# Optimization experiments

Measured on AMD Instinct MI355X. Metric: run time of the kernel, lower is better.

Reference implementation:

```python
import jax, jax.numpy as jnp
import numpy as np

IN_C, HID, OUT_C = 768, 568, 1024
EPS = 1e-5

def _ln(x, g, b):
    mu = jnp.mean(x, axis=-1, keepdims=True)
    var = jnp.var(x, axis=-1, keepdims=True)
    return (x - mu) / jnp.sqrt(var + EPS) * g + b

def setup_inputs() -> dict:
    key = jax.random.key(0)
    ks = jax.random.split(key, 20)
    def lin(k, fan_in, fan_out):
        bound = 1.0 / np.sqrt(fan_in)
        kw, kb = jax.random.split(k)
        w = jax.random.uniform(kw, (fan_in, fan_out), jnp.float32, -bound, bound)
        b = jax.random.uniform(kb, (fan_out,), jnp.float32, -bound, bound)
        return w, b
    x = jax.random.normal(ks[0], (4, 2048, IN_C), jnp.float32)
    w_mlp, b_mlp = lin(ks[1], IN_C, HID)
    wq, bq = lin(ks[2], HID, OUT_C)
    wk, bk = lin(ks[3], HID, OUT_C)
    wv, bv = lin(ks[4], HID, OUT_C)
    wm, bm = lin(ks[5], HID, OUT_C)
    wf1, bf1 = lin(ks[6], OUT_C, OUT_C)
    wf2, bf2 = lin(ks[7], OUT_C, OUT_C)
    g1 = jnp.ones((OUT_C,), jnp.float32); be1 = jnp.zeros((OUT_C,), jnp.float32)
    g2 = jnp.ones((OUT_C,), jnp.float32); be2 = jnp.zeros((OUT_C,), jnp.float32)
    return dict(x=x, w_mlp=w_mlp, b_mlp=b_mlp, wq=wq, bq=bq, wk=wk, bk=bk,
                wv=wv, bv=bv, wm=wm, bm=bm, g1=g1, be1=be1,
                wf1=wf1, bf1=bf1, wf2=wf2, bf2=bf2, g2=g2, be2=be2)

def reference(x, w_mlp, b_mlp, wq, bq, wk, bk, wv, bv, wm, bm,
              g1, be1, wf1, bf1, wf2, bf2, g2, be2):
    # Joint.mlp: Linear + ReLU  -> h: [B, S, HID]
    h = jax.nn.relu(jnp.einsum('bsi,ih->bsh', x, w_mlp) + b_mlp)
    # Block: single-head attention (dropout=eval -> identity)
    q = jnp.einsum('bsh,hd->bsd', h, wq) + bq
    k = jnp.einsum('bsh,hd->bsd', h, wk) + bk
    v = jnp.einsum('bsh,hd->bsd', h, wv) + bv
    scale = 1.0 / jnp.sqrt(jnp.float32(OUT_C))
    attn = jax.nn.softmax(jnp.einsum('bqd,bkd->bqk', q, k) * scale, axis=-1)
    attn_out = jnp.einsum('bqk,bkd->bqd', attn, v)
    x_mod = jnp.einsum('bsh,hd->bsd', h, wm) + bm
    x1 = _ln(x_mod + attn_out, g1, be1)
    ffn = jnp.einsum('bsd,de->bse', jax.nn.relu(jnp.einsum('bsd,de->bse', x1, wf1) + bf1), wf2) + bf2
    x2 = _ln(x1 + ffn, g2, be2)
    # trailing ReLU in Joint.attn Sequential
    return jax.nn.relu(x2)
```

## Files before the change

### kernel.cpp

```cpp
#include <hip/hip_runtime.h>

#define DI __device__ __forceinline__

typedef unsigned short u16;
typedef __attribute__((__ext_vector_type__(8))) __bf16 bf16x8;
typedef __attribute__((__ext_vector_type__(4))) float f32x4;
typedef __attribute__((__ext_vector_type__(4))) unsigned short u16x4;
typedef __attribute__((__ext_vector_type__(8))) unsigned short u16x8;

DI float bf2f(u16 u) { union { unsigned int i; float f; } x; x.i = ((unsigned int)u) << 16; return x.f; }
DI u16 f2bf(float f) {
  union { float f; unsigned int i; } x; x.f = f;
  unsigned int r = x.i + 0x7fffu + ((x.i >> 16) & 1u);
  return (u16)(r >> 16);
}

DI void gload_lds16(const void* g, void* lds) {
  __builtin_amdgcn_global_load_lds((const __attribute__((address_space(1))) unsigned int*)g,
                                   (__attribute__((address_space(3))) unsigned int*)lds, 16, 0, 0);
}

#define MFMA16(a, b, c) __builtin_amdgcn_mfma_f32_16x16x32_bf16((a), (b), (c), 0, 0, 0)

template<bool RELU, bool OUT_BF16, bool HAS_BIAS>
__global__ __launch_bounds__(512, 2)
void gemm256v2(const u16* __restrict__ A, long long sAb, int lda,
               const u16* __restrict__ Bt, long long sBb, int ldb,
               const float* __restrict__ bias,
               void* __restrict__ C, long long sCb, int ldc,
               int K, float scale)
{
  extern __shared__ __align__(16) u16 lds[];

  const int tid = threadIdx.x;
  const int w = tid >> 6, l = tid & 63;
  const int wm = w >> 2, wn = w & 3;

  const int gx = gridDim.x;
  const int nwg = gx * gridDim.y;
  const int f = blockIdx.x + gx * blockIdx.y;
  const int fs = (f & 7) * (nwg >> 3) + (f >> 3);
  const int bx = fs % gx, by = fs / gx;

  const long long bm = (long long)by * 256;
  const long long bn = (long long)bx * 256;
  const u16* Ab = A + (long long)blockIdx.z * sAb;
  const u16* Btb = Bt + (long long)blockIdx.z * sBb;

  const int trow = tid >> 3;
  const int tg = (tid & 7) ^ (trow & 7);
  const u16* sA = Ab + (bm + trow) * (long long)lda + tg * 8;
  const u16* sB = Btb + (bn + trow) * (long long)ldb + tg * 8;
  const long long la64 = (long long)64 * lda, lb64 = (long long)64 * ldb;

  const int swz0 = (((l >> 4) ^ (l & 7))) * 8;
  const int aB = (wm * 128 + (l & 15)) * 64;
  const int bB = 16384 + (wn * 64 + (l & 15)) * 64;

  f32x4 acc[8][4] = {};
  const int NKT = K >> 6;

  {
    u16* sp = lds;
    gload_lds16(sA, sp + w * 512);
    gload_lds16(sA + 2 * la64, sp + 8192 + w * 512);
    gload_lds16(sB, sp + 16384 + w * 512);
    gload_lds16(sB + lb64, sp + 20480 + w * 512);
    gload_lds16(sB + 2 * lb64, sp + 24576 + w * 512);
    gload_lds16(sB + 3 * lb64, sp + 28672 + w * 512);
    gload_lds16(sA + la64, sp + 4096 + w * 512);
    gload_lds16(sA + 3 * la64, sp + 12288 + w * 512);
  }

  for (int kt = 0; kt < NKT; ++kt) {
    const u16* bp = lds + (kt & 1) * 32768;
    u16* sp = lds + ((kt & 1) ^ 1) * 32768;
    const bool st = (kt + 1) < NKT;
    const long long ko = (long long)(kt + 1) * 64;

    asm volatile("s_waitcnt vmcnt(2)" ::: "memory");
    __builtin_amdgcn_s_barrier();

    if (st) {
      gload_lds16(sA + ko, sp + w * 512);
      gload_lds16(sA + 2 * la64 + ko, sp + 8192 + w * 512);
      gload_lds16(sB + ko, sp + 16384 + w * 512);
      gload_lds16(sB + lb64 + ko, sp + 20480 + w * 512);
      gload_lds16(sB + 2 * lb64 + ko, sp + 24576 + w * 512);
      gload_lds16(sB + 3 * lb64 + ko, sp + 28672 + w * 512);
    }

    bf16x8 bF[4][2], aF[4][2];
    #pragma unroll
    for (int nf = 0; nf < 4; ++nf) {
      bF[nf][0] = *(const bf16x8*)(bp + bB + nf * 1024 + swz0);
      bF[nf][1] = *(const bf16x8*)(bp + bB + nf * 1024 + (swz0 ^ 32));
    }
    #pragma unroll
    for (int mf = 0; mf < 4; ++mf) {
      aF[mf][0] = *(const bf16x8*)(bp + aB + mf * 1024 + swz0);
      aF[mf][1] = *(const bf16x8*)(bp + aB + mf * 1024 + (swz0 ^ 32));
    }
    if (st) {
      gload_lds16(sA + la64 + ko, sp + 4096 + w * 512);
      gload_lds16(sA + 3 * la64 + ko, sp + 12288 + w * 512);
    }
    __builtin_amdgcn_s_setprio(1);
    #pragma unroll
    for (int mf = 0; mf < 4; ++mf)
      #pragma unroll
      for (int nf = 0; nf < 4; ++nf) {
        acc[mf][nf] = MFMA16(aF[mf][0], bF[nf][0], acc[mf][nf]);
        acc[mf][nf] = MFMA16(aF[mf][1], bF[nf][1], acc[mf][nf]);
      }
    __builtin_amdgcn_s_setprio(0);

    if (st) asm volatile("s_waitcnt vmcnt(8)" ::: "memory");
    else    asm volatile("s_waitcnt vmcnt(0)" ::: "memory");
    __builtin_amdgcn_s_barrier();

    #pragma unroll
    for (int mf = 0; mf < 4; ++mf) {
      aF[mf][0] = *(const bf16x8*)(bp + aB + (mf + 4) * 1024 + swz0);
      aF[mf][1] = *(const bf16x8*)(bp + aB + (mf + 4) * 1024 + (swz0 ^ 32));
    }
    __builtin_amdgcn_s_setprio(1);
    #pragma unroll
    for (int mf = 0; mf < 4; ++mf)
      #pragma unroll
      for (int nf = 0; nf < 4; ++nf) {
        acc[mf + 4][nf] = MFMA16(aF[mf][0], bF[nf][0], acc[mf + 4][nf]);
        acc[mf + 4][nf] = MFMA16(aF[mf][1], bF[nf][1], acc[mf + 4][nf]);
      }
    __builtin_amdgcn_s_setprio(0);
  }

  __syncthreads();
  float bias4[4];
  if (HAS_BIAS) {
    #pragma unroll
    for (int nf = 0; nf < 4; ++nf) bias4[nf] = bias[bn + wn * 64 + (l & 15) + nf * 16];
  }
  float* fl = (float*)lds + w * 1024;
  const long long cbase = (long long)blockIdx.z * sCb;
  const int q = l >> 4;
  #pragma unroll
  for (int mf = 0; mf < 8; ++mf) {
    #pragma unroll
    for (int nf = 0; nf < 4; ++nf) {
      #pragma unroll
      for (int r = 0; r < 4; ++r) {
        float v = acc[mf][nf][r] * scale;
        if (HAS_BIAS) v += bias4[nf];
        if (RELU) v = fmaxf(v, 0.f);
        fl[(q * 4 + r) * 64 + ((((l & 15) + nf * 16)) ^ (q << 4))] = v;
      }
    }
    asm volatile("s_waitcnt lgkmcnt(0)" ::: "memory");
    #pragma unroll
    for (int p = 0; p < 4; ++p) {
      f32x4 v = *(const f32x4*)(fl + (p * 4 + q) * 64 + (((l & 15) * 4) ^ (p << 4)));
      const long long row = bm + wm * 128 + mf * 16 + p * 4 + q;
      const long long cidx = cbase + row * ldc + bn + wn * 64 + (l & 15) * 4;
      if (OUT_BF16) {
        u16x4 o; o.x = f2bf(v.x); o.y = f2bf(v.y); o.z = f2bf(v.z); o.w = f2bf(v.w);
        *(u16x4*)((u16*)C + cidx) = o;
      } else {
        *(f32x4*)((float*)C + cidx) = v;
      }
    }
    asm volatile("s_waitcnt lgkmcnt(0)" ::: "memory");
  }
}

template<bool RELU, bool OUT_BF16, bool HAS_BIAS>
__global__ __launch_bounds__(512, 4)
void gemm128(const u16* __restrict__ A, long long sAb, int lda,
             const u16* __restrict__ Bt, long long sBb, int ldb,
             const float* __restrict__ bias,
             void* __restrict__ C, long long sCb, int ldc,
             int K, float scale)
{
  __shared__ __align__(16) u16 lds[24576];

  const int tid = threadIdx.x;
  const int w = tid >> 6, l = tid & 63;
  const int wm = w >> 2, wn = w & 3;

  const int gx = gridDim.x;
  const int nwg = gx * gridDim.y;
  const int f = blockIdx.x + gx * blockIdx.y;
  const int fs = (f & 7) * (nwg >> 3) + (f >> 3);
  const int bx = fs % gx, by = fs / gx;

  const long long bm = (long long)by * 128;
  const long long bn = (long long)bx * 256;
  const u16* Ab = A + (long long)blockIdx.z * sAb;
  const u16* Btb = Bt + (long long)blockIdx.z * sBb;

  const int ia = w * 64 + l;
  const int ra = ia >> 2;
  const int ga = (ia & 3) ^ ((ra >> 1) & 3);
  const u16* pA  = Ab  + (bm + ra) * (long long)lda + ga * 8;
  const u16* pB0 = Btb + (bn + ra) * (long long)ldb + ga * 8;
  const u16* pB1 = Btb + (bn + 128 + ra) * (long long)ldb + ga * 8;
  u16* dA  = lds + w * 512;
  u16* dB0 = lds + 4096 + w * 512;
  u16* dB1 = lds + 8192 + w * 512;

  const int swz = ((l >> 4) ^ (((l & 15) >> 1) & 3)) << 3;
  const int aOff = (wm * 64 + (l & 15)) * 32 + swz;
  const int bOff = 4096 + (wn * 64 + (l & 15)) * 32 + swz;

  f32x4 acc[4][4] = {};
  const int NKT = K >> 5;

  gload_lds16(pA, dA);        gload_lds16(pB0, dB0);        gload_lds16(pB1, dB1);
  gload_lds16(pA + 32, dA + 12288); gload_lds16(pB0 + 32, dB0 + 12288); gload_lds16(pB1 + 32, dB1 + 12288);

  for (int kt = 0; kt < NKT; ++kt) {
    if (kt + 1 < NKT) asm volatile("s_waitcnt vmcnt(3)" ::: "memory");
    else              asm volatile("s_waitcnt vmcnt(0)" ::: "memory");
    __builtin_amdgcn_s_barrier();
    __builtin_amdgcn_sched_barrier(0);

    const u16* bufc = lds + (kt & 1) * 12288;
    bf16x8 aF[4], bF[4];
    #pragma unroll
    for (int mf = 0; mf < 4; ++mf) aF[mf] = *(const bf16x8*)(bufc + aOff + mf * 512);
    #pragma unroll
    for (int nf = 0; nf < 4; ++nf) bF[nf] = *(const bf16x8*)(bufc + bOff + nf * 512);
    asm volatile("s_waitcnt lgkmcnt(0)" ::: "memory");
    __builtin_amdgcn_s_barrier();
    __builtin_amdgcn_sched_barrier(0);

    if (kt + 2 < NKT) {
      u16* d = lds + (kt & 1) * 12288 + w * 512;
      const long long ko = (long long)(kt + 2) * 32;
      gload_lds16(pA + ko, d);
      gload_lds16(pB0 + ko, d + 4096);
      gload_lds16(pB1 + ko, d + 8192);
    }
    __builtin_amdgcn_s_setprio(1);
    #pragma unroll
    for (int mf = 0; mf < 4; ++mf)
      #pragma unroll
      for (int nf = 0; nf < 4; ++nf)
        acc[mf][nf] = MFMA16(aF[mf], bF[nf], acc[mf][nf]);
    __builtin_amdgcn_s_setprio(0);
  }

  float bias4[4];
  if (HAS_BIAS) {
    #pragma unroll
    for (int nf = 0; nf < 4; ++nf) bias4[nf] = bias[bn + wn * 64 + (l & 15) + nf * 16];
  }
  float* fl = (float*)lds + w * 1024;
  const long long cbase = (long long)blockIdx.z * sCb;
  const int q = l >> 4;
  #pragma unroll
  for (int mf = 0; mf < 4; ++mf) {
    #pragma unroll
    for (int nf = 0; nf < 4; ++nf) {
      #pragma unroll
      for (int r = 0; r < 4; ++r) {
        float v = acc[mf][nf][r] * scale;
        if (HAS_BIAS) v += bias4[nf];
        if (RELU) v = fmaxf(v, 0.f);
        fl[(q * 4 + r) * 64 + ((((l & 15) + nf * 16)) ^ (q << 4))] = v;
      }
    }
    asm volatile("s_waitcnt lgkmcnt(0)" ::: "memory");
    #pragma unroll
    for (int p = 0; p < 4; ++p) {
      f32x4 v = *(const f32x4*)(fl + (p * 4 + q) * 64 + (((l & 15) * 4) ^ (p << 4)));
      const long long row = bm + wm * 64 + mf * 16 + p * 4 + q;
      const long long cidx = cbase + row * ldc + bn + wn * 64 + (l & 15) * 4;
      if (OUT_BF16) {
        u16x4 o; o.x = f2bf(v.x); o.y = f2bf(v.y); o.z = f2bf(v.z); o.w = f2bf(v.w);
        *(u16x4*)((u16*)C + cidx) = o;
      } else {
        *(f32x4*)((float*)C + cidx) = v;
      }
    }
    asm volatile("s_waitcnt lgkmcnt(0)" ::: "memory");
  }
}

__global__ void transpose_cast_pad(const float* __restrict__ in, int inR, int inC,
                                   u16* __restrict__ out, int outR, int outC)
{
  __shared__ float tile[32][33];
  const int c0 = blockIdx.x * 32;
  const int r0 = blockIdx.y * 32;
  const int tx = threadIdx.x, ty = threadIdx.y;
  for (int i = ty; i < 32; i += 8) {
    int r = r0 + i, c = c0 + tx;
    tile[i][tx] = (r < inR && c < inC) ? in[(long long)r * inC + c] : 0.f;
  }
  __syncthreads();
  for (int i = ty; i < 32; i += 8) {
    int orow = c0 + i, ocol = r0 + tx;
    if (orow < outR && ocol < outC)
      out[(long long)orow * outC + ocol] = f2bf(tile[tx][i]);
  }
}

__global__ void transpose_bf16_k(const u16* __restrict__ in, long long sIb, int ldi,
                                 u16* __restrict__ out, long long sOb, int ldo)
{
  __shared__ u16 tile[32][33];
  const u16* inp = in + (long long)blockIdx.z * sIb;
  u16* outp = out + (long long)blockIdx.z * sOb;
  const int r0 = blockIdx.y * 32, c0 = blockIdx.x * 32;
  const int tx = threadIdx.x, ty = threadIdx.y;
  for (int i = ty; i < 32; i += 8)
    tile[i][tx] = inp[(long long)(r0 + i) * ldi + c0 + tx];
  __syncthreads();
  for (int i = ty; i < 32; i += 8)
    outp[(long long)(c0 + i) * ldo + r0 + tx] = tile[tx][i];
}

__global__ void cast_f32_bf16_k(const float* __restrict__ in, u16* __restrict__ out, int n4)
{
  int i = blockIdx.x * blockDim.x + threadIdx.x;
  if (i >= n4) return;
  float4 v = ((const float4*)in)[i];
  u16x4 o; o.x = f2bf(v.x); o.y = f2bf(v.y); o.z = f2bf(v.z); o.w = f2bf(v.w);
  ((u16x4*)out)[i] = o;
}

__global__ void prep_bias_k(const float* __restrict__ bmlp, const float* __restrict__ bq,
                            const float* __restrict__ bk, const float* __restrict__ bv,
                            const float* __restrict__ bm,
                            float* __restrict__ outMlp, float* __restrict__ outQkvm)
{
  int i = blockIdx.x * 256 + threadIdx.x;
  if (i < 768) outMlp[i] = (i < 568) ? bmlp[i] : 0.f;
  if (i < 4096) {
    const float* s = (i < 1024) ? bq : (i < 2048) ? bk : (i < 3072) ? bv : bm;
    outQkvm[i] = s[i & 1023];
  }
}

__global__ __launch_bounds__(256)
void softmax_rows_k(u16* __restrict__ sc)
{
  __shared__ float red[8];
  const long long base = (long long)blockIdx.x * 2048;
  const int t = threadIdx.x, wave = t >> 6, lane = t & 63;
  u16x8 v8 = *((const u16x8*)(sc + base + t * 8));
  float v[8];
  #pragma unroll
  for (int j = 0; j < 8; ++j) v[j] = bf2f(v8[j]);
  float m = v[0];
  #pragma unroll
  for (int j = 1; j < 8; ++j) m = fmaxf(m, v[j]);
  #pragma unroll
  for (int off = 32; off > 0; off >>= 1) m = fmaxf(m, __shfl_xor(m, off, 64));
  if (lane == 0) red[wave] = m;
  __syncthreads();
  m = fmaxf(fmaxf(red[0], red[1]), fmaxf(red[2], red[3]));
  float s = 0.f;
  #pragma unroll
  for (int j = 0; j < 8; ++j) { v[j] = __expf(v[j] - m); s += v[j]; }
  #pragma unroll
  for (int off = 32; off > 0; off >>= 1) s += __shfl_xor(s, off, 64);
  if (lane == 0) red[4 + wave] = s;
  __syncthreads();
  s = red[4] + red[5] + red[6] + red[7];
  float inv = 1.f / s;
  u16x8 o;
  #pragma unroll
  for (int j = 0; j < 8; ++j) o[j] = f2bf(v[j] * inv);
  *((u16x8*)(sc + base + t * 8)) = o;
}

__global__ __launch_bounds__(256)
void add_ln_k(const u16* __restrict__ a, int lda, const u16* __restrict__ b,
              const float* __restrict__ gamma, const float* __restrict__ beta,
              u16* __restrict__ out)
{
  __shared__ float red[8];
  const long long row = blockIdx.x;
  const int t = threadIdx.x, wave = t >> 6, lane = t & 63;
  u16x4 av = *((const u16x4*)(a + row * lda + t * 4));
  u16x4 bv = *((const u16x4*)(b + row * 1024 + t * 4));
  float z[4] = { bf2f(av.x) + bf2f(bv.x), bf2f(av.y) + bf2f(bv.y),
                 bf2f(av.z) + bf2f(bv.z), bf2f(av.w) + bf2f(bv.w) };
  float s = z[0] + z[1] + z[2] + z[3];
  float ss = z[0]*z[0] + z[1]*z[1] + z[2]*z[2] + z[3]*z[3];
  #pragma unroll
  for (int off = 32; off > 0; off >>= 1) { s += __shfl_xor(s, off, 64); ss += __shfl_xor(ss, off, 64); }
  if (lane == 0) { red[wave] = s; red[4 + wave] = ss; }
  __syncthreads();
  s = red[0] + red[1] + red[2] + red[3];
  ss = red[4] + red[5] + red[6] + red[7];
  float mu = s * (1.f / 1024.f);
  float var = ss * (1.f / 1024.f) - mu * mu;
  float rstd = rsqrtf(var + 1e-5f);
  float4 g = ((const float4*)gamma)[t];
  float4 be = ((const float4*)beta)[t];
  u16x4 o;
  o.x = f2bf((z[0] - mu) * rstd * g.x + be.x);
  o.y = f2bf((z[1] - mu) * rstd * g.y + be.y);
  o.z = f2bf((z[2] - mu) * rstd * g.z + be.z);
  o.w = f2bf((z[3] - mu) * rstd * g.w + be.w);
  *((u16x4*)(out + row * 1024 + t * 4)) = o;
}

__global__ __launch_bounds__(256)
void add_ln_relu_k(const u16* __restrict__ a, const u16* __restrict__ b,
                   const float* __restrict__ gamma, const float* __restrict__ beta,
                   float* __restrict__ out)
{
  __shared__ float red[8];
  const long long row = blockIdx.x;
  const int t = threadIdx.x, wave = t >> 6, lane = t & 63;
  u16x4 av = *((const u16x4*)(a + row * 1024 + t * 4));
  u16x4 bv = *((const u16x4*)(b + row * 1024 + t * 4));
  float z[4] = { bf2f(av.x) + bf2f(bv.x), bf2f(av.y) + bf2f(bv.y),
                 bf2f(av.z) + bf2f(bv.z), bf2f(av.w) + bf2f(bv.w) };
  float s = z[0] + z[1] + z[2] + z[3];
  float ss = z[0]*z[0] + z[1]*z[1] + z[2]*z[2] + z[3]*z[3];
  #pragma unroll
  for (int off = 32; off > 0; off >>= 1) { s += __shfl_xor(s, off, 64); ss += __shfl_xor(ss, off, 64); }
  if (lane == 0) { red[wave] = s; red[4 + wave] = ss; }
  __syncthreads();
  s = red[0] + red[1] + red[2] + red[3];
  ss = red[4] + red[5] + red[6] + red[7];
  float mu = s * (1.f / 1024.f);
  float var = ss * (1.f / 1024.f) - mu * mu;
  float rstd = rsqrtf(var + 1e-5f);
  float4 g = ((const float4*)gamma)[t];
  float4 be = ((const float4*)beta)[t];
  float4 o;
  o.x = fmaxf((z[0] - mu) * rstd * g.x + be.x, 0.f);
  o.y = fmaxf((z[1] - mu) * rstd * g.y + be.y, 0.f);
  o.z = fmaxf((z[2] - mu) * rstd * g.z + be.z, 0.f);
  o.w = fmaxf((z[3] - mu) * rstd * g.w + be.w, 0.f);
  ((float4*)(out + row * 1024))[t] = o;
}

extern "C" void kernel_launch(void* const* d_in, const int* in_sizes, int n_in,
                              void* d_out, int out_size, void* d_ws, size_t ws_size,
                              hipStream_t stream)
{
  const float* x    = (const float*)d_in[0];
  const float* wmlp = (const float*)d_in[1];
  const float* bmlp = (const float*)d_in[2];
  const float* wq   = (const float*)d_in[3];  const float* bq  = (const float*)d_in[4];
  const float* wk   = (const float*)d_in[5];  const float* bk  = (const float*)d_in[6];
  const float* wv   = (const float*)d_in[7];  const float* bv  = (const float*)d_in[8];
  const float* wm   = (const float*)d_in[9];  const float* bm  = (const float*)d_in[10];
  const float* g1   = (const float*)d_in[11]; const float* be1 = (const float*)d_in[12];
  const float* wf1  = (const float*)d_in[13]; const float* bf1 = (const float*)d_in[14];
  const float* wf2  = (const float*)d_in[15]; const float* bf2 = (const float*)d_in[16];
  const float* g2   = (const float*)d_in[17]; const float* be2 = (const float*)d_in[18];

  char* ws = (char*)d_ws;
  size_t off = 0;
  auto alloc = [&](size_t bytes) { char* p = ws + off; off += (bytes + 255) & ~(size_t)255; return p; };
  u16*  W_MLP_T  = (u16*)alloc((size_t)768 * 768 * 2);
  u16*  W_QKVM_T = (u16*)alloc((size_t)4096 * 640 * 2);
  u16*  W_F1_T   = (u16*)alloc((size_t)1024 * 1024 * 2);
  u16*  W_F2_T   = (u16*)alloc((size_t)1024 * 1024 * 2);
  float* B_MLP   = (float*)alloc(768 * 4);
  float* B_QKVM  = (float*)alloc(4096 * 4);
  u16*  XBF      = (u16*)alloc((size_t)8192 * 768 * 2);
  u16*  H        = (u16*)alloc((size_t)8192 * 768 * 2);
  u16*  QKVM     = (u16*)alloc((size_t)8192 * 4096 * 2);
  u16*  VT       = (u16*)alloc((size_t)4 * 1024 * 2048 * 2);
  u16*  SC       = (u16*)alloc((size_t)4 * 2048 * 2048 * 2);
  u16*  AO       = (u16*)alloc((size_t)8192 * 1024 * 2);
  u16*  X1       = (u16*)alloc((size_t)8192 * 1024 * 2);
  u16*  T  = QKVM;
  u16*  F  = QKVM + (size_t)8192 * 1024;

  hipFuncSetAttribute((const void*)gemm256v2<false, true, true >, hipFuncAttributeMaxDynamicSharedMemorySize, 131072);
  hipFuncSetAttribute((const void*)gemm256v2<false, true, false>, hipFuncAttributeMaxDynamicSharedMemorySize, 131072);

  dim3 tb(32, 8);

  cast_f32_bf16_k<<<(8192 * 768 / 4 + 255) / 256, 256, 0, stream>>>(x, XBF, 8192 * 768 / 4);
  transpose_cast_pad<<<dim3(24, 24), tb, 0, stream>>>(wmlp, 768, 568, W_MLP_T, 768, 768);
  transpose_cast_pad<<<dim3(32, 20), tb, 0, stream>>>(wq, 568, 1024, W_QKVM_T + (size_t)0 * 1024 * 640, 1024, 640);
  transpose_cast_pad<<<dim3(32, 20), tb, 0, stream>>>(wk, 568, 1024, W_QKVM_T + (size_t)1 * 1024 * 640, 1024, 640);
  transpose_cast_pad<<<dim3(32, 20), tb, 0, stream>>>(wv, 568, 1024, W_QKVM_T + (size_t)2 * 1024 * 640, 1024, 640);
  transpose_cast_pad<<<dim3(32, 20), tb, 0, stream>>>(wm, 568, 1024, W_QKVM_T + (size_t)3 * 1024 * 640, 1024, 640);
  transpose_cast_pad<<<dim3(32, 32), tb, 0, stream>>>(wf1, 1024, 1024, W_F1_T, 1024, 1024);
  transpose_cast_pad<<<dim3(32, 32), tb, 0, stream>>>(wf2, 1024, 1024, W_F2_T, 1024, 1024);
  prep_bias_k<<<16, 256, 0, stream>>>(bmlp, bq, bk, bv, bm, B_MLP, B_QKVM);

  gemm128<true, true, true><<<dim3(3, 64, 1), 512, 0, stream>>>(
      XBF, 0, 768, W_MLP_T, 0, 768, B_MLP, H, 0, 768, 768, 1.0f);
  gemm256v2<false, true, true><<<dim3(16, 32, 1), 512, 131072, stream>>>(
      H, 0, 768, W_QKVM_T, 0, 640, B_QKVM, QKVM, 0, 4096, 640, 1.0f);
  transpose_bf16_k<<<dim3(32, 64, 4), tb, 0, stream>>>(
      QKVM + 2048, (long long)2048 * 4096, 4096, VT, (long long)1024 * 2048, 2048);
  gemm256v2<false, true, false><<<dim3(8, 8, 4), 512, 131072, stream>>>(
      QKVM, (long long)2048 * 4096, 4096, QKVM + 1024, (long long)2048 * 4096, 4096,
      nullptr, SC, (long long)2048 * 2048, 2048, 1024, 0.03125f);
  softmax_rows_k<<<8192, 256, 0, stream>>>(SC);
  gemm128<false, true, false><<<dim3(4, 16, 4), 512, 0, stream>>>(
      SC, (long long)2048 * 2048, 2048, VT, (long long)1024 * 2048, 2048,
      nullptr, AO, (long long)2048 * 1024, 1024, 2048, 1.0f);
  add_ln_k<<<8192, 256, 0, stream>>>(QKVM + 3072, 4096, AO, g1, be1, X1);
  gemm128<true, true, true><<<dim3(4, 64, 1), 512, 0, stream>>>(
      X1, 0, 1024, W_F1_T, 0, 1024, bf1, T, 0, 1024, 1024, 1.0f);
  gemm128<false, true, true><<<dim3(4, 64, 1), 512, 0, stream>>>(
      T, 0, 1024, W_F2_T, 0, 1024, bf2, F, 0, 1024, 1024, 1.0f);
  add_ln_relu_k<<<8192, 256, 0, stream>>>(X1, F, g2, be2, (float*)d_out);
}
```

Measured before the change: 271.9 us.

## Restructure 256x256 GEMM into 8-phase quadrant schedule with interleaved half-tile loads

```diff
diff --git a/kernel.cpp b/kernel.cpp
--- a/kernel.cpp
+++ b/kernel.cpp
@@ -24,11 +24,11 @@
 
 template<bool RELU, bool OUT_BF16, bool HAS_BIAS>
 __global__ __launch_bounds__(512, 2)
-void gemm256v2(const u16* __restrict__ A, long long sAb, int lda,
-               const u16* __restrict__ Bt, long long sBb, int ldb,
-               const float* __restrict__ bias,
-               void* __restrict__ C, long long sCb, int ldc,
-               int K, float scale)
+void gemm8q(const u16* __restrict__ A, long long sAb, int lda,
+            const u16* __restrict__ Bt, long long sBb, int ldb,
+            const float* __restrict__ bias,
+            void* __restrict__ C, long long sCb, int ldc,
+            int K, float scale)
 {
   extern __shared__ __align__(16) u16 lds[];
 
@@ -49,101 +49,101 @@
 
   const int trow = tid >> 3;
   const int tg = (tid & 7) ^ (trow & 7);
-  const u16* sA = Ab + (bm + trow) * (long long)lda + tg * 8;
-  const u16* sB = Btb + (bn + trow) * (long long)ldb + tg * 8;
-  const long long la64 = (long long)64 * lda, lb64 = (long long)64 * ldb;
-
-  const int swz0 = (((l >> 4) ^ (l & 7))) * 8;
-  const int aB = (wm * 128 + (l & 15)) * 64;
-  const int bB = 16384 + (wn * 64 + (l & 15)) * 64;
+  const u16* gA = Ab + (bm + trow) * (long long)lda + tg * 8;
+  const u16* gB = Btb + (bn + trow) * (long long)ldb + tg * 8;
+
+#define STG(gP, ld, h, t, dOff) { \
+    const u16* s_ = (gP) + (long long)((h) * 128) * (ld) + (long long)(t) * 64; \
+    u16* d_ = lds + (dOff) + w * 512; \
+    gload_lds16(s_, d_); \
+    gload_lds16(s_ + (long long)64 * (ld), d_ + 4096); }
+#define STAGE_A(t, h, buf) STG(gA, lda, h, t, (buf) * 32768 + (h) * 8192)
+#define STAGE_B(t, h, buf) STG(gB, ldb, h, t, (buf) * 32768 + 16384 + (h) * 8192)
+
+  const int slotX = ((l >> 4) ^ (l & 7)) * 8;
+  const int aRowB = (wm * 64 + (l & 15)) * 64 + slotX;
+  const int bRowB = (wn * 32 + (l & 15)) * 64 + slotX;
+  const int aLoOff = aRowB;
+  const int aHiOff = 8192 + aRowB;
+  const int bLoOff = 16384 + bRowB;
+  const int bHiOff = 24576 + bRowB;
+
+#define RD_A(base) { _Pragma("unroll") for (int mf = 0; mf < 4; ++mf) { \
+    aF[mf][0] = *(const bf16x8*)(lds + ((base) + mf * 1024)); \
+    aF[mf][1] = *(const bf16x8*)(lds + (((base) + mf * 1024) ^ 32)); } }
+#define RD_B(dst, base) { _Pragma("unroll") for (int nf = 0; nf < 2; ++nf) { \
+    dst[nf][0] = *(const bf16x8*)(lds + ((base) + nf * 1024)); \
+    dst[nf][1] = *(const bf16x8*)(lds + (((base) + nf * 1024) ^ 32)); } }
+#define QUAD(MO, NO, B) { _Pragma("unroll") for (int mf = 0; mf < 4; ++mf) { \
+    _Pragma("unroll") for (int nf = 0; nf < 2; ++nf) { \
+      acc[mf + MO][nf + NO] = MFMA16(aF[mf][0], B[nf][0], acc[mf + MO][nf + NO]); \
+      acc[mf + MO][nf + NO] = MFMA16(aF[mf][1], B[nf][1], acc[mf + MO][nf + NO]); } } }
+#define PH_MID() \
+    __builtin_amdgcn_s_barrier(); \
+    asm volatile("s_waitcnt lgkmcnt(0)" ::: "memory"); \
+    __builtin_amdgcn_sched_barrier(0); \
+    __builtin_amdgcn_s_setprio(1);
+#define PH_END() \
+    __builtin_amdgcn_s_setprio(0); \
+    __builtin_amdgcn_s_barrier();
 
   f32x4 acc[8][4] = {};
+  bf16x8 aF[4][2], bLo[2][2], bHi[2][2];
   const int NKT = K >> 6;
-
-  {
-    u16* sp = lds;
-    gload_lds16(sA, sp + w * 512);
-    gload_lds16(sA + 2 * la64, sp + 8192 + w * 512);
-    gload_lds16(sB, sp + 16384 + w * 512);
-    gload_lds16(sB + lb64, sp + 20480 + w * 512);
-    gload_lds16(sB + 2 * lb64, sp + 24576 + w * 512);
-    gload_lds16(sB + 3 * lb64, sp + 28672 + w * 512);
-    gload_lds16(sA + la64, sp + 4096 + w * 512);
-    gload_lds16(sA + 3 * la64, sp + 12288 + w * 512);
-  }
-
-  for (int kt = 0; kt < NKT; ++kt) {
-    const u16* bp = lds + (kt & 1) * 32768;
-    u16* sp = lds + ((kt & 1) ^ 1) * 32768;
-    const bool st = (kt + 1) < NKT;
-    const long long ko = (long long)(kt + 1) * 64;
-
-    asm volatile("s_waitcnt vmcnt(2)" ::: "memory");
-    __builtin_amdgcn_s_barrier();
-
-    if (st) {
-      gload_lds16(sA + ko, sp + w * 512);
-      gload_lds16(sA + 2 * la64 + ko, sp + 8192 + w * 512);
-      gload_lds16(sB + ko, sp + 16384 + w * 512);
-      gload_lds16(sB + lb64 + ko, sp + 20480 + w * 512);
-      gload_lds16(sB + 2 * lb64 + ko, sp + 24576 + w * 512);
-      gload_lds16(sB + 3 * lb64 + ko, sp + 28672 + w * 512);
-    }
-
-    bf16x8 bF[4][2], aF[4][2];
-    #pragma unroll
-    for (int nf = 0; nf < 4; ++nf) {
-      bF[nf][0] = *(const bf16x8*)(bp + bB + nf * 1024 + swz0);
-      bF[nf][1] = *(const bf16x8*)(bp + bB + nf * 1024 + (swz0 ^ 32));
-    }
-    #pragma unroll
-    for (int mf = 0; mf < 4; ++mf) {
-      aF[mf][0] = *(const bf16x8*)(bp + aB + mf * 1024 + swz0);
-      aF[mf][1] = *(const bf16x8*)(bp + aB + mf * 1024 + (swz0 ^ 32));
-    }
-    if (st) {
-      gload_lds16(sA + la64 + ko, sp + 4096 + w * 512);
-      gload_lds16(sA + 3 * la64 + ko, sp + 12288 + w * 512);
-    }
-    __builtin_amdgcn_s_setprio(1);
-    #pragma unroll
-    for (int mf = 0; mf < 4; ++mf)
-      #pragma unroll
-      for (int nf = 0; nf < 4; ++nf) {
-        acc[mf][nf] = MFMA16(aF[mf][0], bF[nf][0], acc[mf][nf]);
-        acc[mf][nf] = MFMA16(aF[mf][1], bF[nf][1], acc[mf][nf]);
-      }
-    __builtin_amdgcn_s_setprio(0);
-
-    if (st) asm volatile("s_waitcnt vmcnt(8)" ::: "memory");
+  const int NIT = NKT >> 1;
+
+  STAGE_A(0, 0, 0); STAGE_A(0, 1, 0); STAGE_B(0, 0, 0); STAGE_B(0, 1, 0);
+  STAGE_A(1, 0, 1); STAGE_B(1, 0, 1); STAGE_B(1, 1, 1);
+  asm volatile("s_waitcnt vmcnt(6)" ::: "memory");
+  __builtin_amdgcn_s_barrier();
+
+  for (int i = 0; i < NIT; ++i) {
+    const bool go = (i + 1) < NIT;
+    const int btile = 2 * i + 1, c = 2 * i + 2, d = 2 * i + 3;
+
+    RD_A(aLoOff); RD_B(bLo, bLoOff);
+    STAGE_A(btile, 1, 1);
+    PH_MID(); QUAD(0, 0, bLo); PH_END();
+    RD_B(bHi, bHiOff);
+    if (go) STAGE_A(c, 0, 0);
+    PH_MID(); QUAD(0, 2, bHi); PH_END();
+    RD_A(aHiOff);
+    if (go) STAGE_B(c, 0, 0);
+    PH_MID(); QUAD(4, 2, bHi); PH_END();
+    if (go) STAGE_B(c, 1, 0);
+    if (go) asm volatile("s_waitcnt vmcnt(6)" ::: "memory");
     else    asm volatile("s_waitcnt vmcnt(0)" ::: "memory");
-    __builtin_amdgcn_s_barrier();
-
-    #pragma unroll
-    for (int mf = 0; mf < 4; ++mf) {
-      aF[mf][0] = *(const bf16x8*)(bp + aB + (mf + 4) * 1024 + swz0);
-      aF[mf][1] = *(const bf16x8*)(bp + aB + (mf + 4) * 1024 + (swz0 ^ 32));
-    }
-    __builtin_amdgcn_s_setprio(1);
-    #pragma unroll
-    for (int mf = 0; mf < 4; ++mf)
-      #pragma unroll
-      for (int nf = 0; nf < 4; ++nf) {
-        acc[mf + 4][nf] = MFMA16(aF[mf][0], bF[nf][0], acc[mf + 4][nf]);
-        acc[mf + 4][nf] = MFMA16(aF[mf][1], bF[nf][1], acc[mf + 4][nf]);
-      }
-    __builtin_amdgcn_s_setprio(0);
+    PH_MID(); QUAD(4, 0, bLo); PH_END();
+
+    RD_A(32768 + aLoOff); RD_B(bLo, 32768 + bLoOff);
+    if (go) STAGE_A(c, 1, 0);
+    PH_MID(); QUAD(0, 0, bLo); PH_END();
+    RD_B(bHi, 32768 + bHiOff);
+    if (go) STAGE_A(d, 0, 1);
+    PH_MID(); QUAD(0, 2, bHi); PH_END();
+    RD_A(32768 + aHiOff);
+    if (go) STAGE_B(d, 0, 1);
+    PH_MID(); QUAD(4, 2, bHi); PH_END();
+    if (go) STAGE_B(d, 1, 1);
+    if (go) asm volatile("s_waitcnt vmcnt(6)" ::: "memory");
+    else    asm volatile("s_waitcnt vmcnt(0)" ::: "memory");
+    PH_MID(); QUAD(4, 0, bLo); PH_END();
   }
 
   __syncthreads();
   float bias4[4];
   if (HAS_BIAS) {
     #pragma unroll
-    for (int nf = 0; nf < 4; ++nf) bias4[nf] = bias[bn + wn * 64 + (l & 15) + nf * 16];
+    for (int nf = 0; nf < 4; ++nf) {
+      const int pc = (nf < 2) ? (wn * 32 + nf * 16) : (128 + wn * 32 + (nf - 2) * 16);
+      bias4[nf] = bias[bn + pc + (l & 15)];
+    }
   }
   float* fl = (float*)lds + w * 1024;
   const long long cbase = (long long)blockIdx.z * sCb;
   const int q = l >> 4;
+  const int cl = (l & 15) * 4;
+  const int physcol = (cl < 32) ? (wn * 32 + cl) : (128 + wn * 32 + (cl - 32));
   #pragma unroll
   for (int mf = 0; mf < 8; ++mf) {
     #pragma unroll
@@ -157,11 +157,12 @@
       }
     }
     asm volatile("s_waitcnt lgkmcnt(0)" ::: "memory");
+    const int rowb = (mf < 4) ? (wm * 64 + mf * 16) : (128 + wm * 64 + (mf - 4) * 16);
     #pragma unroll
     for (int p = 0; p < 4; ++p) {
-      f32x4 v = *(const f32x4*)(fl + (p * 4 + q) * 64 + (((l & 15) * 4) ^ (p << 4)));
-      const long long row = bm + wm * 128 + mf * 16 + p * 4 + q;
-      const long long cidx = cbase + row * ldc + bn + wn * 64 + (l & 15) * 4;
+      f32x4 v = *(const f32x4*)(fl + (p * 4 + q) * 64 + (cl ^ (p << 4)));
+      const long long row = bm + rowb + p * 4 + q;
+      const long long cidx = cbase + row * ldc + bn + physcol;
       if (OUT_BF16) {
         u16x4 o; o.x = f2bf(v.x); o.y = f2bf(v.y); o.z = f2bf(v.z); o.w = f2bf(v.w);
         *(u16x4*)((u16*)C + cidx) = o;
@@ -171,6 +172,14 @@
     }
     asm volatile("s_waitcnt lgkmcnt(0)" ::: "memory");
   }
+#undef STG
+#undef STAGE_A
+#undef STAGE_B
+#undef RD_A
+#undef RD_B
+#undef QUAD
+#undef PH_MID
+#undef PH_END
 }
 
 template<bool RELU, bool OUT_BF16, bool HAS_BIAS>
@@ -477,8 +486,8 @@
   u16*  T  = QKVM;
   u16*  F  = QKVM + (size_t)8192 * 1024;
 
-  hipFuncSetAttribute((const void*)gemm256v2<false, true, true >, hipFuncAttributeMaxDynamicSharedMemorySize, 131072);
-  hipFuncSetAttribute((const void*)gemm256v2<false, true, false>, hipFuncAttributeMaxDynamicSharedMemorySize, 131072);
+  hipFuncSetAttribute((const void*)gemm8q<false, true, true >, hipFuncAttributeMaxDynamicSharedMemorySize, 131072);
+  hipFuncSetAttribute((const void*)gemm8q<false, true, false>, hipFuncAttributeMaxDynamicSharedMemorySize, 131072);
 
   dim3 tb(32, 8);
 
@@ -494,11 +503,11 @@
 
   gemm128<true, true, true><<<dim3(3, 64, 1), 512, 0, stream>>>(
       XBF, 0, 768, W_MLP_T, 0, 768, B_MLP, H, 0, 768, 768, 1.0f);
-  gemm256v2<false, true, true><<<dim3(16, 32, 1), 512, 131072, stream>>>(
+  gemm8q<false, true, true><<<dim3(16, 32, 1), 512, 131072, stream>>>(
       H, 0, 768, W_QKVM_T, 0, 640, B_QKVM, QKVM, 0, 4096, 640, 1.0f);
   transpose_bf16_k<<<dim3(32, 64, 4), tb, 0, stream>>>(
       QKVM + 2048, (long long)2048 * 4096, 4096, VT, (long long)1024 * 2048, 2048);
-  gemm256v2<false, true, false><<<dim3(8, 8, 4), 512, 131072, stream>>>(
+  gemm8q<false, true, false><<<dim3(8, 8, 4), 512, 131072, stream>>>(
       QKVM, (long long)2048 * 4096, 4096, QKVM + 1024, (long long)2048 * 4096, 4096,
       nullptr, SC, (long long)2048 * 2048, 2048, 1024, 0.03125f);
   softmax_rows_k<<<8192, 256, 0, stream>>>(SC);
```

Result: no change. 274.9 us (+1.1%).

## Replace 128x256 GEMM with 256x128 BK64 kernel and vectorize V transpose

Applied to the files above, without the earlier changes.

```diff
diff --git a/kernel.cpp b/kernel.cpp
--- a/kernel.cpp
+++ b/kernel.cpp
@@ -174,14 +174,14 @@
 }
 
 template<bool RELU, bool OUT_BF16, bool HAS_BIAS>
-__global__ __launch_bounds__(512, 4)
-void gemm128(const u16* __restrict__ A, long long sAb, int lda,
-             const u16* __restrict__ Bt, long long sBb, int ldb,
-             const float* __restrict__ bias,
-             void* __restrict__ C, long long sCb, int ldc,
-             int K, float scale)
-{
-  __shared__ __align__(16) u16 lds[24576];
+__global__ __launch_bounds__(512, 2)
+void gemm256n128(const u16* __restrict__ A, long long sAb, int lda,
+                 const u16* __restrict__ Bt, long long sBb, int ldb,
+                 const float* __restrict__ bias,
+                 void* __restrict__ C, long long sCb, int ldc,
+                 int K, float scale)
+{
+  extern __shared__ __align__(16) u16 lds[];
 
   const int tid = threadIdx.x;
   const int w = tid >> 6, l = tid & 63;
@@ -193,89 +193,121 @@
   const int fs = (f & 7) * (nwg >> 3) + (f >> 3);
   const int bx = fs % gx, by = fs / gx;
 
-  const long long bm = (long long)by * 128;
-  const long long bn = (long long)bx * 256;
+  const long long bm = (long long)by * 256;
+  const long long bn = (long long)bx * 128;
   const u16* Ab = A + (long long)blockIdx.z * sAb;
   const u16* Btb = Bt + (long long)blockIdx.z * sBb;
 
-  const int ia = w * 64 + l;
-  const int ra = ia >> 2;
-  const int ga = (ia & 3) ^ ((ra >> 1) & 3);
-  const u16* pA  = Ab  + (bm + ra) * (long long)lda + ga * 8;
-  const u16* pB0 = Btb + (bn + ra) * (long long)ldb + ga * 8;
-  const u16* pB1 = Btb + (bn + 128 + ra) * (long long)ldb + ga * 8;
-  u16* dA  = lds + w * 512;
-  u16* dB0 = lds + 4096 + w * 512;
-  u16* dB1 = lds + 8192 + w * 512;
-
-  const int swz = ((l >> 4) ^ (((l & 15) >> 1) & 3)) << 3;
-  const int aOff = (wm * 64 + (l & 15)) * 32 + swz;
-  const int bOff = 4096 + (wn * 64 + (l & 15)) * 32 + swz;
-
-  f32x4 acc[4][4] = {};
-  const int NKT = K >> 5;
-
-  gload_lds16(pA, dA);        gload_lds16(pB0, dB0);        gload_lds16(pB1, dB1);
-  gload_lds16(pA + 32, dA + 12288); gload_lds16(pB0 + 32, dB0 + 12288); gload_lds16(pB1 + 32, dB1 + 12288);
+  const int trow = tid >> 3;
+  const int tg = (tid & 7) ^ (trow & 7);
+  const u16* gA = Ab + (bm + trow) * (long long)lda + tg * 8;
+  const u16* gB = Btb + (bn + trow) * (long long)ldb + tg * 8;
+  const long long la64 = (long long)64 * lda, lb64 = (long long)64 * ldb;
+
+  const int swz0 = ((l >> 4) ^ (l & 7)) * 8;
+  const int aB = (wm * 128 + (l & 15)) * 64;
+  const int bB = 16384 + (wn * 32 + (l & 15)) * 64;
+
+  f32x4 acc[8][2] = {};
+  const int NKT = K >> 6;
+
+  gload_lds16(gA,            lds + w * 512);
+  gload_lds16(gA + 2 * la64, lds + 8192 + w * 512);
+  gload_lds16(gB,            lds + 16384 + w * 512);
+  gload_lds16(gB + lb64,     lds + 20480 + w * 512);
+  gload_lds16(gA + la64,     lds + 4096 + w * 512);
+  gload_lds16(gA + 3 * la64, lds + 12288 + w * 512);
 
   for (int kt = 0; kt < NKT; ++kt) {
-    if (kt + 1 < NKT) asm volatile("s_waitcnt vmcnt(3)" ::: "memory");
-    else              asm volatile("s_waitcnt vmcnt(0)" ::: "memory");
+    const u16* bp = lds + (kt & 1) * 24576;
+    u16* sp = lds + ((kt & 1) ^ 1) * 24576;
+    const bool st = (kt + 1) < NKT;
+    const long long ko = (long long)(kt + 1) * 64;
+
+    asm volatile("s_waitcnt vmcnt(2)" ::: "memory");
     __builtin_amdgcn_s_barrier();
-    __builtin_amdgcn_sched_barrier(0);
-
-    const u16* bufc = lds + (kt & 1) * 12288;
-    bf16x8 aF[4], bF[4];
-    #pragma unroll
-    for (int mf = 0; mf < 4; ++mf) aF[mf] = *(const bf16x8*)(bufc + aOff + mf * 512);
-    #pragma unroll
-    for (int nf = 0; nf < 4; ++nf) bF[nf] = *(const bf16x8*)(bufc + bOff + nf * 512);
-    asm volatile("s_waitcnt lgkmcnt(0)" ::: "memory");
-    __builtin_amdgcn_s_barrier();
-    __builtin_amdgcn_sched_barrier(0);
-
-    if (kt + 2 < NKT) {
-      u16* d = lds + (kt & 1) * 12288 + w * 512;
-      const long long ko = (long long)(kt + 2) * 32;
-      gload_lds16(pA + ko, d);
-      gload_lds16(pB0 + ko, d + 4096);
-      gload_lds16(pB1 + ko, d + 8192);
+
+    if (st) {
+      gload_lds16(gA + ko,            sp + w * 512);
+      gload_lds16(gA + 2 * la64 + ko, sp + 8192 + w * 512);
+      gload_lds16(gB + ko,            sp + 16384 + w * 512);
+      gload_lds16(gB + lb64 + ko,     sp + 20480 + w * 512);
+    }
+
+    bf16x8 bF[2][2], aF[4][2];
+    #pragma unroll
+    for (int nf = 0; nf < 2; ++nf) {
+      bF[nf][0] = *(const bf16x8*)(bp + bB + nf * 1024 + swz0);
+      bF[nf][1] = *(const bf16x8*)(bp + bB + nf * 1024 + (swz0 ^ 32));
+    }
+    #pragma unroll
+    for (int mf = 0; mf < 4; ++mf) {
+      aF[mf][0] = *(const bf16x8*)(bp + aB + mf * 1024 + swz0);
+      aF[mf][1] = *(const bf16x8*)(bp + aB + mf * 1024 + (swz0 ^ 32));
+    }
+    if (st) {
+      gload_lds16(gA + la64 + ko,     sp + 4096 + w * 512);
+      gload_lds16(gA + 3 * la64 + ko, sp + 12288 + w * 512);
     }
     __builtin_amdgcn_s_setprio(1);
     #pragma unroll
     for (int mf = 0; mf < 4; ++mf)
       #pragma unroll
-      for (int nf = 0; nf < 4; ++nf)
-        acc[mf][nf] = MFMA16(aF[mf], bF[nf], acc[mf][nf]);
+      for (int nf = 0; nf < 2; ++nf) {
+        acc[mf][nf] = MFMA16(aF[mf][0], bF[nf][0], acc[mf][nf]);
+        acc[mf][nf] = MFMA16(aF[mf][1], bF[nf][1], acc[mf][nf]);
+      }
     __builtin_amdgcn_s_setprio(0);
-  }
-
-  float bias4[4];
+
+    if (st) asm volatile("s_waitcnt vmcnt(6)" ::: "memory");
+    else    asm volatile("s_waitcnt vmcnt(0)" ::: "memory");
+    __builtin_amdgcn_s_barrier();
+
+    #pragma unroll
+    for (int mf = 0; mf < 4; ++mf) {
+      aF[mf][0] = *(const bf16x8*)(bp + aB + (mf + 4) * 1024 + swz0);
+      aF[mf][1] = *(const bf16x8*)(bp + aB + (mf + 4) * 1024 + (swz0 ^ 32));
+    }
+    __builtin_amdgcn_s_setprio(1);
+    #pragma unroll
+    for (int mf = 0; mf < 4; ++mf)
+      #pragma unroll
+      for (int nf = 0; nf < 2; ++nf) {
+        acc[mf + 4][nf] = MFMA16(aF[mf][0], bF[nf][0], acc[mf + 4][nf]);
+        acc[mf + 4][nf] = MFMA16(aF[mf][1], bF[nf][1], acc[mf + 4][nf]);
+      }
+    __builtin_amdgcn_s_setprio(0);
+  }
+
+  __syncthreads();
+  float bias2[2];
   if (HAS_BIAS) {
     #pragma unroll
-    for (int nf = 0; nf < 4; ++nf) bias4[nf] = bias[bn + wn * 64 + (l & 15) + nf * 16];
-  }
-  float* fl = (float*)lds + w * 1024;
+    for (int nf = 0; nf < 2; ++nf) bias2[nf] = bias[bn + wn * 32 + (l & 15) + nf * 16];
+  }
+  float* fl = (float*)lds + w * 512;
   const long long cbase = (long long)blockIdx.z * sCb;
   const int q = l >> 4;
   #pragma unroll
-  for (int mf = 0; mf < 4; ++mf) {
-    #pragma unroll
-    for (int nf = 0; nf < 4; ++nf) {
+  for (int mf = 0; mf < 8; ++mf) {
+    #pragma unroll
+    for (int nf = 0; nf < 2; ++nf) {
       #pragma unroll
       for (int r = 0; r < 4; ++r) {
         float v = acc[mf][nf][r] * scale;
-        if (HAS_BIAS) v += bias4[nf];
+        if (HAS_BIAS) v += bias2[nf];
         if (RELU) v = fmaxf(v, 0.f);
-        fl[(q * 4 + r) * 64 + ((((l & 15) + nf * 16)) ^ (q << 4))] = v;
+        fl[(q * 4 + r) * 32 + ((((l & 15) + nf * 16)) ^ ((q & 1) << 4))] = v;
       }
     }
     asm volatile("s_waitcnt lgkmcnt(0)" ::: "memory");
     #pragma unroll
-    for (int p = 0; p < 4; ++p) {
-      f32x4 v = *(const f32x4*)(fl + (p * 4 + q) * 64 + (((l & 15) * 4) ^ (p << 4)));
-      const long long row = bm + wm * 64 + mf * 16 + p * 4 + q;
-      const long long cidx = cbase + row * ldc + bn + wn * 64 + (l & 15) * 4;
+    for (int p = 0; p < 2; ++p) {
+      const int orow = p * 8 + (l >> 3);
+      const int X = ((orow >> 2) & 1) << 4;
+      f32x4 v = *(const f32x4*)(fl + orow * 32 + (((l & 7) * 4) ^ X));
+      const long long row = bm + wm * 128 + mf * 16 + orow;
+      const long long cidx = cbase + row * ldc + bn + wn * 32 + (l & 7) * 4;
       if (OUT_BF16) {
         u16x4 o; o.x = f2bf(v.x); o.y = f2bf(v.y); o.z = f2bf(v.z); o.w = f2bf(v.w);
         *(u16x4*)((u16*)C + cidx) = o;
@@ -306,19 +338,31 @@
   }
 }
 
-__global__ void transpose_bf16_k(const u16* __restrict__ in, long long sIb, int ldi,
-                                 u16* __restrict__ out, long long sOb, int ldo)
-{
-  __shared__ u16 tile[32][33];
+__global__ __launch_bounds__(256)
+void transpose64_k(const u16* __restrict__ in, long long sIb, int ldi,
+                   u16* __restrict__ out, long long sOb, int ldo)
+{
+  __shared__ u16 tile[64][72];
   const u16* inp = in + (long long)blockIdx.z * sIb;
   u16* outp = out + (long long)blockIdx.z * sOb;
-  const int r0 = blockIdx.y * 32, c0 = blockIdx.x * 32;
-  const int tx = threadIdx.x, ty = threadIdx.y;
-  for (int i = ty; i < 32; i += 8)
-    tile[i][tx] = inp[(long long)(r0 + i) * ldi + c0 + tx];
-  __syncthreads();
-  for (int i = ty; i < 32; i += 8)
-    outp[(long long)(c0 + i) * ldo + r0 + tx] = tile[tx][i];
+  const int r0 = blockIdx.y * 64, c0 = blockIdx.x * 64;
+  const int t = threadIdx.x;
+  const int jr = t >> 3, ch = t & 7;
+  #pragma unroll
+  for (int it = 0; it < 2; ++it) {
+    const int row = jr + it * 32;
+    u16x8 v = *(const u16x8*)(inp + (long long)(r0 + row) * ldi + c0 + ch * 8);
+    *(u16x8*)(&tile[row][ch * 8]) = v;
+  }
+  __syncthreads();
+  #pragma unroll
+  for (int it = 0; it < 2; ++it) {
+    const int orow = jr + it * 32;
+    u16x8 v;
+    #pragma unroll
+    for (int e = 0; e < 8; ++e) v[e] = tile[ch * 8 + e][orow];
+    *(u16x8*)(outp + (long long)(c0 + orow) * ldo + r0 + ch * 8) = v;
+  }
 }
 
 __global__ void cast_f32_bf16_k(const float* __restrict__ in, u16* __restrict__ out, int n4)
@@ -479,6 +523,9 @@
 
   hipFuncSetAttribute((const void*)gemm256v2<false, true, true >, hipFuncAttributeMaxDynamicSharedMemorySize, 131072);
   hipFuncSetAttribute((const void*)gemm256v2<false, true, false>, hipFuncAttributeMaxDynamicSharedMemorySize, 131072);
+  hipFuncSetAttribute((const void*)gemm256n128<true,  true, true >, hipFuncAttributeMaxDynamicSharedMemorySize, 98304);
+  hipFuncSetAttribute((const void*)gemm256n128<false, true, false>, hipFuncAttributeMaxDynamicSharedMemorySize, 98304);
+  hipFuncSetAttribute((const void*)gemm256n128<false, true, true >, hipFuncAttributeMaxDynamicSharedMemorySize, 98304);
 
   dim3 tb(32, 8);
 
@@ -492,23 +539,23 @@
   transpose_cast_pad<<<dim3(32, 32), tb, 0, stream>>>(wf2, 1024, 1024, W_F2_T, 1024, 1024);
   prep_bias_k<<<16, 256, 0, stream>>>(bmlp, bq, bk, bv, bm, B_MLP, B_QKVM);
 
-  gemm128<true, true, true><<<dim3(3, 64, 1), 512, 0, stream>>>(
+  gemm256n128<true, true, true><<<dim3(6, 32, 1), 512, 98304, stream>>>(
       XBF, 0, 768, W_MLP_T, 0, 768, B_MLP, H, 0, 768, 768, 1.0f);
   gemm256v2<false, true, true><<<dim3(16, 32, 1), 512, 131072, stream>>>(
       H, 0, 768, W_QKVM_T, 0, 640, B_QKVM, QKVM, 0, 4096, 640, 1.0f);
-  transpose_bf16_k<<<dim3(32, 64, 4), tb, 0, stream>>>(
+  transpose64_k<<<dim3(16, 32, 4), 256, 0, stream>>>(
       QKVM + 2048, (long long)2048 * 4096, 4096, VT, (long long)1024 * 2048, 2048);
   gemm256v2<false, true, false><<<dim3(8, 8, 4), 512, 131072, stream>>>(
       QKVM, (long long)2048 * 4096, 4096, QKVM + 1024, (long long)2048 * 4096, 4096,
       nullptr, SC, (long long)2048 * 2048, 2048, 1024, 0.03125f);
   softmax_rows_k<<<8192, 256, 0, stream>>>(SC);
-  gemm128<false, true, false><<<dim3(4, 16, 4), 512, 0, stream>>>(
+  gemm256n128<false, true, false><<<dim3(8, 8, 4), 512, 98304, stream>>>(
       SC, (long long)2048 * 2048, 2048, VT, (long long)1024 * 2048, 2048,
       nullptr, AO, (long long)2048 * 1024, 1024, 2048, 1.0f);
   add_ln_k<<<8192, 256, 0, stream>>>(QKVM + 3072, 4096, AO, g1, be1, X1);
-  gemm128<true, true, true><<<dim3(4, 64, 1), 512, 0, stream>>>(
+  gemm256n128<true, true, true><<<dim3(8, 32, 1), 512, 98304, stream>>>(
       X1, 0, 1024, W_F1_T, 0, 1024, bf1, T, 0, 1024, 1024, 1.0f);
-  gemm128<false, true, true><<<dim3(4, 64, 1), 512, 0, stream>>>(
+  gemm256n128<false, true, true><<<dim3(8, 32, 1), 512, 98304, stream>>>(
       T, 0, 1024, W_F2_T, 0, 1024, bf2, F, 0, 1024, 1024, 1.0f);
   add_ln_relu_k<<<8192, 256, 0, stream>>>(X1, F, g2, be2, (float*)d_out);
 }
```

New measurement: 253.4 us. 6.8% less time.
